# Kernel tuning notes

Measured on AMD Instinct MI355X. Metric: run time of the kernel, lower is better.

## Reference

```python
import jax, jax.numpy as jnp
import numpy as np

H, KV, DH = 16, 4, 64  # num_heads, num_kv_heads, head_dim


def setup_inputs() -> dict:
    key = jax.random.key(0)
    k1, k2, k3, k4, k5 = jax.random.split(key, 5)
    B, L, D = 1, 4096, 1024
    s = 0.02
    return {
        "x": jax.random.normal(k1, (B, L, D), dtype=jnp.float32),
        "Wq": jax.random.normal(k2, (D, H * DH), dtype=jnp.float32) * s,
        "Wk": jax.random.normal(k3, (D, KV * DH), dtype=jnp.float32) * s,
        "Wv": jax.random.normal(k4, (D, KV * DH), dtype=jnp.float32) * s,
        "Wo": jax.random.normal(k5, (H * DH, D), dtype=jnp.float32) * s,
    }


def _rotate_half(t):
    t1, t2 = t[..., : DH // 2], t[..., DH // 2 :]
    return jnp.concatenate([-t2, t1], axis=-1)


def reference(x, Wq, Wk, Wv, Wo):
    B, L, D = x.shape
    G = H // KV  # query heads per kv head
    q = (x @ Wq).reshape(B, L, H, DH)
    k = (x @ Wk).reshape(B, L, KV, DH)
    v = (x @ Wv).reshape(B, L, KV, DH)

    # RoPE: inv_freq over even dims, angles duplicated across both halves
    inv_freq = 1.0 / (10000.0 ** (jnp.arange(0, DH, 2, dtype=jnp.float32) / DH))
    t = jnp.arange(L, dtype=jnp.float32)
    freqs = t[:, None] * inv_freq[None, :]                 # [L, DH/2]
    emb = jnp.concatenate([freqs, freqs], axis=-1)[None, :, None, :]  # [1,L,1,DH]
    cos, sin = jnp.cos(emb), jnp.sin(emb)
    q = q * cos + _rotate_half(q) * sin
    k = k * cos + _rotate_half(k) * sin

    # GQA: query head h attends with kv head h // G (repeat_interleave layout)
    qg = q.reshape(B, L, KV, G, DH)
    scale = DH ** -0.5
    attn = jnp.einsum("bqkgd,bskd->bkgqs", qg, k) * scale  # [B,KV,G,L,L]
    attn = jax.nn.softmax(attn, axis=-1)
    out = jnp.einsum("bkgqs,bskd->bqkgd", attn, v).reshape(B, L, H * DH)
    return out @ Wo
```

## Files before the change

### kernel.cpp

```cpp
#include <hip/hip_runtime.h>
#include <math.h>

#define L 4096
#define D 1024
#define H 16
#define KV 4
#define DH 64

typedef __attribute__((ext_vector_type(8))) short bf16x8;
typedef __attribute__((ext_vector_type(4))) float f32x4;

static __device__ __forceinline__ unsigned short f2bf(float f) {
    unsigned u = __float_as_uint(f);
    u = (u + 0x7FFF + ((u >> 16) & 1)) >> 16;
    return (unsigned short)u;
}

#define EXP2F(x) __builtin_amdgcn_exp2f(x)

#define GLD16(src, dst) \
    __builtin_amdgcn_global_load_lds((__attribute__((address_space(1))) void*)(src), \
                                     (__attribute__((address_space(3))) void*)(dst), 16, 0, 0)

__global__ __launch_bounds__(256) void prep_kernel(
        const float* __restrict__ x,  const float* __restrict__ Wq,
        const float* __restrict__ Wk, const float* __restrict__ Wv,
        const float* __restrict__ Wo,
        unsigned short* __restrict__ xb, unsigned short* __restrict__ WqkvT,
        unsigned short* __restrict__ WoT) {
    const int b = blockIdx.x, tid = threadIdx.x;
    if (b < 4096) {
        int i = (b * 256 + tid) * 4;
        float4 v = *(const float4*)&x[i];
        ushort4 o;
        o.x = f2bf(v.x); o.y = f2bf(v.y); o.z = f2bf(v.z); o.w = f2bf(v.w);
        *(ushort4*)&xb[i] = o;
        return;
    }
    __shared__ float t[32][33];
    const float* src; unsigned short* dst; int N, n0, k0;
    if (b < 5120)      { int tq = b - 4096; src = Wq; dst = WqkvT;                     N = 1024; n0 = (tq & 31) * 32; k0 = (tq >> 5) * 32; }
    else if (b < 5376) { int tq = b - 5120; src = Wk; dst = WqkvT + (size_t)1024*1024; N = 256;  n0 = (tq & 7)  * 32; k0 = (tq >> 3) * 32; }
    else if (b < 5632) { int tq = b - 5376; src = Wv; dst = WqkvT + (size_t)1280*1024; N = 256;  n0 = (tq & 7)  * 32; k0 = (tq >> 3) * 32; }
    else               { int tq = b - 5632; src = Wo; dst = WoT;                       N = 1024; n0 = (tq & 31) * 32; k0 = (tq >> 5) * 32; }
    const int tx = tid & 31, ty = tid >> 5;
    #pragma unroll
    for (int j = 0; j < 4; ++j)
        t[ty + 8 * j][tx] = src[(size_t)(k0 + ty + 8 * j) * N + n0 + tx];
    __syncthreads();
    #pragma unroll
    for (int j = 0; j < 4; ++j)
        dst[(size_t)(n0 + ty + 8 * j) * 1024 + k0 + tx] = f2bf(t[tx][ty + 8 * j]);
}

__global__ __launch_bounds__(256) void gemm_bf16(const unsigned short* __restrict__ A,
                                                 const unsigned short* __restrict__ BT,
                                                 float* __restrict__ C,
                                                 int M, int N, int K) {
    __shared__ unsigned short As[128 * 32];
    __shared__ unsigned short Bs[128 * 32];

    const int tid  = threadIdx.x;
    const int w    = tid >> 6;
    const int lane = tid & 63;
    const int c    = lane & 15;
    const int quad = lane >> 4;
    const int wy = w >> 1, wx = w & 1;
    const int row0 = blockIdx.y * 128;
    const int col0 = blockIdx.x * 128;

    const int ld_row = w * 16 + (lane >> 2);
    const int ld_col = (lane & 3) * 8;

    f32x4 acc[4][4];
    #pragma unroll
    for (int mt = 0; mt < 4; ++mt)
        #pragma unroll
        for (int nt = 0; nt < 4; ++nt)
            acc[mt][nt] = (f32x4){0.f, 0.f, 0.f, 0.f};

    for (int k0 = 0; k0 < K; k0 += 32) {
        __syncthreads();
        GLD16(&A [(size_t)(row0 + ld_row)      * K + k0 + ld_col], &As[w * 512]);
        GLD16(&A [(size_t)(row0 + ld_row + 64) * K + k0 + ld_col], &As[w * 512 + 2048]);
        GLD16(&BT[(size_t)(col0 + ld_row)      * K + k0 + ld_col], &Bs[w * 512]);
        GLD16(&BT[(size_t)(col0 + ld_row + 64) * K + k0 + ld_col], &Bs[w * 512 + 2048]);
        __syncthreads();

        bf16x8 af[4], bfr[4];
        #pragma unroll
        for (int mt = 0; mt < 4; ++mt)
            af[mt] = *(const bf16x8*)&As[(wy * 64 + mt * 16 + c) * 32 + quad * 8];
        #pragma unroll
        for (int nt = 0; nt < 4; ++nt)
            bfr[nt] = *(const bf16x8*)&Bs[(wx * 64 + nt * 16 + c) * 32 + quad * 8];

        #pragma unroll
        for (int mt = 0; mt < 4; ++mt)
            #pragma unroll
            for (int nt = 0; nt < 4; ++nt)
                acc[mt][nt] = __builtin_amdgcn_mfma_f32_16x16x32_bf16(af[mt], bfr[nt], acc[mt][nt], 0, 0, 0);
    }

    #pragma unroll
    for (int mt = 0; mt < 4; ++mt)
        #pragma unroll
        for (int nt = 0; nt < 4; ++nt)
            #pragma unroll
            for (int r = 0; r < 4; ++r)
                C[(size_t)(row0 + wy * 64 + mt * 16 + quad * 4 + r) * N
                  + col0 + wx * 64 + nt * 16 + c] = acc[mt][nt][r];
}

__global__ __launch_bounds__(256) void gemm_qkv_rope(
        const unsigned short* __restrict__ A,
        const unsigned short* __restrict__ BT,
        unsigned short* __restrict__ qb,
        unsigned short* __restrict__ kbuf,
        unsigned short* __restrict__ vbuf) {
    __shared__ unsigned short As[128 * 32];
    __shared__ unsigned short Bs[128 * 32];

    const int tid  = threadIdx.x;
    const int w    = tid >> 6;
    const int lane = tid & 63;
    const int c    = lane & 15;
    const int quad = lane >> 4;
    const int wy = w >> 1, wx = w & 1;
    const int row0 = blockIdx.y * 128;
    const int col0 = blockIdx.x * 128;

    const int ld_row = w * 16 + (lane >> 2);
    const int ld_col = (lane & 3) * 8;

    f32x4 acc[4][4];
    #pragma unroll
    for (int mt = 0; mt < 4; ++mt)
        #pragma unroll
        for (int nt = 0; nt < 4; ++nt)
            acc[mt][nt] = (f32x4){0.f, 0.f, 0.f, 0.f};

    for (int k0 = 0; k0 < 1024; k0 += 32) {
        __syncthreads();
        GLD16(&A [(size_t)(row0 + ld_row)      * 1024 + k0 + ld_col], &As[w * 512]);
        GLD16(&A [(size_t)(row0 + ld_row + 64) * 1024 + k0 + ld_col], &As[w * 512 + 2048]);
        GLD16(&BT[(size_t)(col0 + ld_row)      * 1024 + k0 + ld_col], &Bs[w * 512]);
        GLD16(&BT[(size_t)(col0 + ld_row + 64) * 1024 + k0 + ld_col], &Bs[w * 512 + 2048]);
        __syncthreads();

        bf16x8 af[4], bfr[4];
        #pragma unroll
        for (int mt = 0; mt < 4; ++mt)
            af[mt] = *(const bf16x8*)&As[(wy * 64 + mt * 16 + c) * 32 + quad * 8];
        #pragma unroll
        for (int nt = 0; nt < 4; ++nt)
            bfr[nt] = *(const bf16x8*)&Bs[(wx * 64 + nt * 16 + c) * 32 + quad * 8];

        #pragma unroll
        for (int mt = 0; mt < 4; ++mt)
            #pragma unroll
            for (int nt = 0; nt < 4; ++nt)
                acc[mt][nt] = __builtin_amdgcn_mfma_f32_16x16x32_bf16(af[mt], bfr[nt], acc[mt][nt], 0, 0, 0);
    }

    const int colb = col0 + wx * 64;
    if (colb < 1280) {
        unsigned short* dst; int hh, hstride; float scale;
        if (colb < 1024) { dst = qb;   hh = colb >> 6;          hstride = H;  scale = 0.18033688011112042f; }
        else             { dst = kbuf; hh = (colb - 1024) >> 6; hstride = KV; scale = 1.0f; }
        #pragma unroll
        for (int nt = 0; nt < 2; ++nt) {
            int d = nt * 16 + c;
            float invf = EXP2F((float)d * -0.4152410118609203f);
            #pragma unroll
            for (int mt = 0; mt < 4; ++mt)
                #pragma unroll
                for (int r = 0; r < 4; ++r) {
                    int l = row0 + wy * 64 + mt * 16 + quad * 4 + r;
                    float ang = (float)l * invf;
                    float sn = __sinf(ang), cs = __cosf(ang);
                    float x1 = acc[mt][nt][r], x2 = acc[mt][nt + 2][r];
                    dst[((size_t)l * hstride + hh) * DH + d]      = f2bf((x1 * cs - x2 * sn) * scale);
                    dst[((size_t)l * hstride + hh) * DH + d + 32] = f2bf((x2 * cs + x1 * sn) * scale);
                }
        }
    } else {
        int vh = (colb - 1280) >> 6;
        #pragma unroll
        for (int mt = 0; mt < 4; ++mt)
            #pragma unroll
            for (int nt = 0; nt < 4; ++nt)
                #pragma unroll
                for (int r = 0; r < 4; ++r) {
                    int l = row0 + wy * 64 + mt * 16 + quad * 4 + r;
                    vbuf[((size_t)l * KV + vh) * DH + nt * 16 + c] = f2bf(acc[mt][nt][r]);
                }
    }
}

__global__ __launch_bounds__(512, 2) void attn_mfma_kernel(
        const unsigned short* __restrict__ qb,
        const unsigned short* __restrict__ kb,
        const unsigned short* __restrict__ vb,
        unsigned short* __restrict__ ob) {
    __shared__ __align__(16) unsigned short Vt[2][2][64][64];
    __shared__ __align__(16) unsigned short Ps[8][64][64];

    const int tid  = threadIdx.x;
    const int w    = tid >> 6;
    const int lane = tid & 63;
    const int c    = lane & 15;
    const int quad = lane >> 4;
    const int g    = w >> 2;
    const int kv = blockIdx.y;
    const int h  = kv * 4 + (w & 3);
    const int q0 = blockIdx.x * 64;
    const int s_base = g * 2048;

    bf16x8 qfrag[4][2];
    #pragma unroll
    for (int qt = 0; qt < 4; ++qt)
        #pragma unroll
        for (int kt = 0; kt < 2; ++kt)
            qfrag[qt][kt] = *(const bf16x8*)&qb[((size_t)(q0 + qt * 16 + c) * H + h) * DH
                                                + kt * 32 + quad * 8];

    f32x4 oacc[4][4];
    f32x4 oones[4];
    #pragma unroll
    for (int qt = 0; qt < 4; ++qt) {
        oones[qt] = (f32x4){0.f, 0.f, 0.f, 0.f};
        #pragma unroll
        for (int dt = 0; dt < 4; ++dt)
            oacc[qt][dt] = (f32x4){0.f, 0.f, 0.f, 0.f};
    }
    const short one_bf = (short)0x3F80;
    const bf16x8 ones8 = {one_bf, one_bf, one_bf, one_bf, one_bf, one_bf, one_bf, one_bf};

    const int tid8 = tid & 255;
    const int sp = tid8 & 31, dc = tid8 >> 5;
    unsigned short* PsW = &Ps[w][0][0];
    const int xr = c & 7;

    int4 vreg0 = *(const int4*)&vb[((size_t)(s_base + 2 * sp)     * KV + kv) * DH + dc * 8];
    int4 vreg1 = *(const int4*)&vb[((size_t)(s_base + 2 * sp + 1) * KV + kv) * DH + dc * 8];
    bf16x8 kA[4][2], kB[4][2];
    #pragma unroll
    for (int mt = 0; mt < 4; ++mt)
        #pragma unroll
        for (int kt = 0; kt < 2; ++kt)
            kA[mt][kt] = *(const bf16x8*)&kb[((size_t)(s_base + mt * 16 + c) * KV + kv) * DH + kt * 32 + quad * 8];

    auto step = [&](int it, int buf, bf16x8 kc[4][2], bf16x8 kn[4][2]) {
        {
            const unsigned* pa = (const unsigned*)&vreg0;
            const unsigned* pb = (const unsigned*)&vreg1;
            #pragma unroll
            for (int t = 0; t < 4; ++t) {
                unsigned lo = __builtin_amdgcn_perm(pb[t], pa[t], 0x05040100u);
                unsigned hi = __builtin_amdgcn_perm(pb[t], pa[t], 0x07060302u);
                int dl = dc * 8 + 2 * t, dh = dl + 1;
                *(unsigned*)&Vt[g][buf][dl][(((sp >> 2) ^ (dl & 7)) << 3) + 2 * (sp & 3)] = lo;
                *(unsigned*)&Vt[g][buf][dh][(((sp >> 2) ^ (dh & 7)) << 3) + 2 * (sp & 3)] = hi;
            }
        }
        __syncthreads();

        int s1 = s_base + ((it + 1) & 31) * 64;
        vreg0 = *(const int4*)&vb[((size_t)(s1 + 2 * sp)     * KV + kv) * DH + dc * 8];
        vreg1 = *(const int4*)&vb[((size_t)(s1 + 2 * sp + 1) * KV + kv) * DH + dc * 8];
        #pragma unroll
        for (int mt = 0; mt < 4; ++mt)
            #pragma unroll
            for (int kt = 0; kt < 2; ++kt)
                kn[mt][kt] = *(const bf16x8*)&kb[((size_t)(s1 + mt * 16 + c) * KV + kv) * DH + kt * 32 + quad * 8];

        #pragma unroll
        for (int mt = 0; mt < 4; ++mt) {
            f32x4 st[4];
            #pragma unroll
            for (int qt = 0; qt < 4; ++qt) {
                f32x4 a = (f32x4){0.f, 0.f, 0.f, 0.f};
                a = __builtin_amdgcn_mfma_f32_16x16x32_bf16(kc[mt][0], qfrag[qt][0], a, 0, 0, 0);
                a = __builtin_amdgcn_mfma_f32_16x16x32_bf16(kc[mt][1], qfrag[qt][1], a, 0, 0, 0);
                st[qt] = a;
            }
            #pragma unroll
            for (int qt = 0; qt < 4; ++qt) {
                float p0 = EXP2F(st[qt][0]);
                float p1 = EXP2F(st[qt][1]);
                float p2 = EXP2F(st[qt][2]);
                float p3 = EXP2F(st[qt][3]);
                uint2 pk;
                pk.x = __builtin_amdgcn_perm(__float_as_uint(p1), __float_as_uint(p0), 0x07060302u);
                pk.y = __builtin_amdgcn_perm(__float_as_uint(p3), __float_as_uint(p2), 0x07060302u);
                *(uint2*)&PsW[(qt * 16 + c) * 64 + (((2 * mt + (quad >> 1)) ^ xr) << 3) + (quad & 1) * 4] = pk;
            }
        }

        bf16x8 pf[4][2];
        #pragma unroll
        for (int qt = 0; qt < 4; ++qt)
            #pragma unroll
            for (int kt = 0; kt < 2; ++kt)
                pf[qt][kt] = *(const bf16x8*)&PsW[(qt * 16 + c) * 64 + (((kt * 4 + quad) ^ xr) << 3)];

        #pragma unroll
        for (int dt = 0; dt < 4; ++dt) {
            bf16x8 vf0 = *(const bf16x8*)&Vt[g][buf][dt * 16 + c][((0 * 4 + quad) ^ xr) << 3];
            bf16x8 vf1 = *(const bf16x8*)&Vt[g][buf][dt * 16 + c][((1 * 4 + quad) ^ xr) << 3];
            #pragma unroll
            for (int qt = 0; qt < 4; ++qt) {
                oacc[qt][dt] = __builtin_amdgcn_mfma_f32_16x16x32_bf16(pf[qt][0], vf0, oacc[qt][dt], 0, 0, 0);
                oacc[qt][dt] = __builtin_amdgcn_mfma_f32_16x16x32_bf16(pf[qt][1], vf1, oacc[qt][dt], 0, 0, 0);
            }
        }
        #pragma unroll
        for (int qt = 0; qt < 4; ++qt) {
            oones[qt] = __builtin_amdgcn_mfma_f32_16x16x32_bf16(pf[qt][0], ones8, oones[qt], 0, 0, 0);
            oones[qt] = __builtin_amdgcn_mfma_f32_16x16x32_bf16(pf[qt][1], ones8, oones[qt], 0, 0, 0);
        }
    };

    for (int it = 0; it < 32; it += 2) {
        step(it,     0, kA, kB);
        step(it + 1, 1, kB, kA);
    }

    __syncthreads();
    if (g == 1) {
        float* dsto = (float*)&Ps[0][0][0] + (size_t)(w - 4) * 4096 + lane * 64;
        #pragma unroll
        for (int qt = 0; qt < 4; ++qt)
            #pragma unroll
            for (int dt = 0; dt < 4; ++dt)
                *(f32x4*)&dsto[qt * 16 + dt * 4] = oacc[qt][dt];
        float* dsts = (float*)&Vt[0][0][0][0] + (size_t)(w - 4) * 1024 + lane * 16;
        #pragma unroll
        for (int qt = 0; qt < 4; ++qt)
            *(f32x4*)&dsts[qt * 4] = oones[qt];
    }
    __syncthreads();
    if (g == 0) {
        const float* srco = (const float*)&Ps[0][0][0] + (size_t)w * 4096 + lane * 64;
        const float* srcs = (const float*)&Vt[0][0][0][0] + (size_t)w * 1024 + lane * 16;
        #pragma unroll
        for (int qt = 0; qt < 4; ++qt) {
            f32x4 po = *(const f32x4*)&srcs[qt * 4];
            oones[qt] += po;
            #pragma unroll
            for (int dt = 0; dt < 4; ++dt)
                oacc[qt][dt] += *(const f32x4*)&srco[qt * 16 + dt * 4];
        }
        #pragma unroll
        for (int qt = 0; qt < 4; ++qt)
            #pragma unroll
            for (int r = 0; r < 4; ++r) {
                float inv = 1.0f / oones[qt][r];
                int row = q0 + qt * 16 + quad * 4 + r;
                #pragma unroll
                for (int dt = 0; dt < 4; ++dt)
                    ob[(size_t)row * (H * DH) + h * DH + dt * 16 + c] = f2bf(oacc[qt][dt][r] * inv);
            }
    }
}

extern "C" void kernel_launch(void* const* d_in, const int* in_sizes, int n_in,
                              void* d_out, int out_size, void* d_ws, size_t ws_size,
                              hipStream_t stream) {
    const float* x  = (const float*)d_in[0];
    const float* Wq = (const float*)d_in[1];
    const float* Wk = (const float*)d_in[2];
    const float* Wv = (const float*)d_in[3];
    const float* Wo = (const float*)d_in[4];
    float* out = (float*)d_out;

    char* ws = (char*)d_ws;
    unsigned short* xb    = (unsigned short*)ws;
    unsigned short* ob    = xb;
    unsigned short* qb    = (unsigned short*)(ws + 8388608);
    unsigned short* kb    = (unsigned short*)(ws + 16777216);
    unsigned short* vb    = (unsigned short*)(ws + 18874368);
    unsigned short* WqkvT = (unsigned short*)(ws + 20971520);
    unsigned short* WoT   = (unsigned short*)(ws + 24117248);

    dim3 blk(256);

    prep_kernel<<<6656, blk, 0, stream>>>(x, Wq, Wk, Wv, Wo, xb, WqkvT, WoT);

    gemm_qkv_rope<<<dim3(12, 32), blk, 0, stream>>>(xb, WqkvT, qb, kb, vb);

    attn_mfma_kernel<<<dim3(L / 64, KV), dim3(512), 0, stream>>>(qb, kb, vb, ob);

    gemm_bf16<<<dim3(D / 128, L / 128), blk, 0, stream>>>(ob, WoT, out, L, D, D);
}
```

Before: 230.0 us.

## Switch attention to 32x32x16 MFMA with register-resident P via permlane32 swap

Rewrites the attention inner loop to use 32x32x16 bf16 MFMA tiles instead of 16x16x32. The exp'd scores are converted to the PV operand layout in registers with permlane32_swap, so the per-wave LDS round trip for P goes away. Row sums are now accumulated with scalar adds instead of extra MFMAs against a ones vector. It also adds s_setprio around the PV MFMAs and reworks the cross-group reduction with a swizzled float LDS buffer. The trade-off is higher register pressure from the 16-wide accumulators, and the softmax denominators are built from truncated bf16 values so they match the numerators used in PV.

```diff
diff --git a/kernel.cpp b/kernel.cpp
--- a/kernel.cpp
+++ b/kernel.cpp
@@ -9,6 +9,8 @@
 
 typedef __attribute__((ext_vector_type(8))) short bf16x8;
 typedef __attribute__((ext_vector_type(4))) float f32x4;
+typedef __attribute__((ext_vector_type(16))) float f32x16;
+typedef __attribute__((ext_vector_type(2))) unsigned int u32x2;
 
 static __device__ __forceinline__ unsigned short f2bf(float f) {
     unsigned u = __float_as_uint(f);
@@ -16,7 +18,14 @@
     return (unsigned short)u;
 }
 
+static __device__ __forceinline__ bf16x8 mk8(unsigned a, unsigned b, unsigned c, unsigned d) {
+    union { unsigned u[4]; bf16x8 v; } x;
+    x.u[0] = a; x.u[1] = b; x.u[2] = c; x.u[3] = d;
+    return x.v;
+}
+
 #define EXP2F(x) __builtin_amdgcn_exp2f(x)
+#define ZERO16 ((f32x16){0.f,0.f,0.f,0.f,0.f,0.f,0.f,0.f,0.f,0.f,0.f,0.f,0.f,0.f,0.f,0.f})
 
 #define GLD16(src, dst) \
     __builtin_amdgcn_global_load_lds((__attribute__((address_space(1))) void*)(src), \
@@ -204,163 +213,183 @@
         const unsigned short* __restrict__ vb,
         unsigned short* __restrict__ ob) {
     __shared__ __align__(16) unsigned short Vt[2][2][64][64];
-    __shared__ __align__(16) unsigned short Ps[8][64][64];
+    __shared__ __align__(16) float Ep[4][64][64];
+    __shared__ __align__(16) float Rs[8][2][32];
 
     const int tid  = threadIdx.x;
     const int w    = tid >> 6;
     const int lane = tid & 63;
-    const int c    = lane & 15;
-    const int quad = lane >> 4;
+    const int c32  = lane & 31;
+    const int hi   = lane >> 5;
     const int g    = w >> 2;
     const int kv = blockIdx.y;
     const int h  = kv * 4 + (w & 3);
     const int q0 = blockIdx.x * 64;
     const int s_base = g * 2048;
 
-    bf16x8 qfrag[4][2];
-    #pragma unroll
-    for (int qt = 0; qt < 4; ++qt)
-        #pragma unroll
-        for (int kt = 0; kt < 2; ++kt)
-            qfrag[qt][kt] = *(const bf16x8*)&qb[((size_t)(q0 + qt * 16 + c) * H + h) * DH
-                                                + kt * 32 + quad * 8];
-
-    f32x4 oacc[4][4];
-    f32x4 oones[4];
-    #pragma unroll
-    for (int qt = 0; qt < 4; ++qt) {
-        oones[qt] = (f32x4){0.f, 0.f, 0.f, 0.f};
-        #pragma unroll
-        for (int dt = 0; dt < 4; ++dt)
-            oacc[qt][dt] = (f32x4){0.f, 0.f, 0.f, 0.f};
-    }
-    const short one_bf = (short)0x3F80;
-    const bf16x8 ones8 = {one_bf, one_bf, one_bf, one_bf, one_bf, one_bf, one_bf, one_bf};
+    bf16x8 qf[2][4];
+    {
+        const unsigned short* qbase = qb + ((size_t)(q0 + c32) * H + h) * DH + hi * 8;
+        #pragma unroll
+        for (int qt = 0; qt < 2; ++qt)
+            #pragma unroll
+            for (int kd = 0; kd < 4; ++kd)
+                qf[qt][kd] = *(const bf16x8*)&qbase[qt * 32 * H * DH + kd * 16];
+    }
+
+    f32x16 oacc[2][2];
+    #pragma unroll
+    for (int qt = 0; qt < 2; ++qt)
+        #pragma unroll
+        for (int dt = 0; dt < 2; ++dt)
+            oacc[qt][dt] = ZERO16;
+    float rsum[2] = {0.f, 0.f};
 
     const int tid8 = tid & 255;
     const int sp = tid8 & 31, dc = tid8 >> 5;
-    unsigned short* PsW = &Ps[w][0][0];
-    const int xr = c & 7;
-
-    int4 vreg0 = *(const int4*)&vb[((size_t)(s_base + 2 * sp)     * KV + kv) * DH + dc * 8];
-    int4 vreg1 = *(const int4*)&vb[((size_t)(s_base + 2 * sp + 1) * KV + kv) * DH + dc * 8];
-    bf16x8 kA[4][2], kB[4][2];
-    #pragma unroll
-    for (int mt = 0; mt < 4; ++mt)
-        #pragma unroll
-        for (int kt = 0; kt < 2; ++kt)
-            kA[mt][kt] = *(const bf16x8*)&kb[((size_t)(s_base + mt * 16 + c) * KV + kv) * DH + kt * 32 + quad * 8];
-
-    auto step = [&](int it, int buf, bf16x8 kc[4][2], bf16x8 kn[4][2]) {
+
+    const unsigned short* kbase = kb + ((size_t)(s_base + c32) * KV + kv) * DH + hi * 8;
+    const unsigned short* vbase = vb + ((size_t)(s_base + 2 * sp) * KV + kv) * DH + dc * 8;
+
+    int4 vreg0 = *(const int4*)&vbase[0];
+    int4 vreg1 = *(const int4*)&vbase[KV * DH];
+    bf16x8 kf[2][4];
+    #pragma unroll
+    for (int a = 0; a < 2; ++a)
+        #pragma unroll
+        for (int kd = 0; kd < 4; ++kd)
+            kf[a][kd] = *(const bf16x8*)&kbase[a * 32 * KV * DH + kd * 16];
+
+    auto step = [&](int it, int buf) {
         {
             const unsigned* pa = (const unsigned*)&vreg0;
             const unsigned* pb = (const unsigned*)&vreg1;
             #pragma unroll
             for (int t = 0; t < 4; ++t) {
                 unsigned lo = __builtin_amdgcn_perm(pb[t], pa[t], 0x05040100u);
-                unsigned hi = __builtin_amdgcn_perm(pb[t], pa[t], 0x07060302u);
-                int dl = dc * 8 + 2 * t, dh = dl + 1;
-                *(unsigned*)&Vt[g][buf][dl][(((sp >> 2) ^ (dl & 7)) << 3) + 2 * (sp & 3)] = lo;
-                *(unsigned*)&Vt[g][buf][dh][(((sp >> 2) ^ (dh & 7)) << 3) + 2 * (sp & 3)] = hi;
+                unsigned hv = __builtin_amdgcn_perm(pb[t], pa[t], 0x07060302u);
+                int dl = dc * 8 + 2 * t, dh2 = dl + 1;
+                *(unsigned*)&Vt[g][buf][dl ][(((sp >> 2) ^ (dl  & 7)) << 3) + 2 * (sp & 3)] = lo;
+                *(unsigned*)&Vt[g][buf][dh2][(((sp >> 2) ^ (dh2 & 7)) << 3) + 2 * (sp & 3)] = hv;
             }
         }
         __syncthreads();
 
-        int s1 = s_base + ((it + 1) & 31) * 64;
-        vreg0 = *(const int4*)&vb[((size_t)(s1 + 2 * sp)     * KV + kv) * DH + dc * 8];
-        vreg1 = *(const int4*)&vb[((size_t)(s1 + 2 * sp + 1) * KV + kv) * DH + dc * 8];
-        #pragma unroll
-        for (int mt = 0; mt < 4; ++mt)
-            #pragma unroll
-            for (int kt = 0; kt < 2; ++kt)
-                kn[mt][kt] = *(const bf16x8*)&kb[((size_t)(s1 + mt * 16 + c) * KV + kv) * DH + kt * 32 + quad * 8];
-
-        #pragma unroll
-        for (int mt = 0; mt < 4; ++mt) {
-            f32x4 st[4];
-            #pragma unroll
-            for (int qt = 0; qt < 4; ++qt) {
-                f32x4 a = (f32x4){0.f, 0.f, 0.f, 0.f};
-                a = __builtin_amdgcn_mfma_f32_16x16x32_bf16(kc[mt][0], qfrag[qt][0], a, 0, 0, 0);
-                a = __builtin_amdgcn_mfma_f32_16x16x32_bf16(kc[mt][1], qfrag[qt][1], a, 0, 0, 0);
-                st[qt] = a;
-            }
-            #pragma unroll
-            for (int qt = 0; qt < 4; ++qt) {
-                float p0 = EXP2F(st[qt][0]);
-                float p1 = EXP2F(st[qt][1]);
-                float p2 = EXP2F(st[qt][2]);
-                float p3 = EXP2F(st[qt][3]);
-                uint2 pk;
-                pk.x = __builtin_amdgcn_perm(__float_as_uint(p1), __float_as_uint(p0), 0x07060302u);
-                pk.y = __builtin_amdgcn_perm(__float_as_uint(p3), __float_as_uint(p2), 0x07060302u);
-                *(uint2*)&PsW[(qt * 16 + c) * 64 + (((2 * mt + (quad >> 1)) ^ xr) << 3) + (quad & 1) * 4] = pk;
-            }
-        }
-
-        bf16x8 pf[4][2];
-        #pragma unroll
-        for (int qt = 0; qt < 4; ++qt)
-            #pragma unroll
-            for (int kt = 0; kt < 2; ++kt)
-                pf[qt][kt] = *(const bf16x8*)&PsW[(qt * 16 + c) * 64 + (((kt * 4 + quad) ^ xr) << 3)];
-
-        #pragma unroll
-        for (int dt = 0; dt < 4; ++dt) {
-            bf16x8 vf0 = *(const bf16x8*)&Vt[g][buf][dt * 16 + c][((0 * 4 + quad) ^ xr) << 3];
-            bf16x8 vf1 = *(const bf16x8*)&Vt[g][buf][dt * 16 + c][((1 * 4 + quad) ^ xr) << 3];
-            #pragma unroll
-            for (int qt = 0; qt < 4; ++qt) {
-                oacc[qt][dt] = __builtin_amdgcn_mfma_f32_16x16x32_bf16(pf[qt][0], vf0, oacc[qt][dt], 0, 0, 0);
-                oacc[qt][dt] = __builtin_amdgcn_mfma_f32_16x16x32_bf16(pf[qt][1], vf1, oacc[qt][dt], 0, 0, 0);
-            }
-        }
-        #pragma unroll
-        for (int qt = 0; qt < 4; ++qt) {
-            oones[qt] = __builtin_amdgcn_mfma_f32_16x16x32_bf16(pf[qt][0], ones8, oones[qt], 0, 0, 0);
-            oones[qt] = __builtin_amdgcn_mfma_f32_16x16x32_bf16(pf[qt][1], ones8, oones[qt], 0, 0, 0);
+        const int itn = (it + 1) & 31;
+        vreg0 = *(const int4*)&vbase[(size_t)itn * 64 * KV * DH];
+        vreg1 = *(const int4*)&vbase[(size_t)itn * 64 * KV * DH + KV * DH];
+
+        #pragma unroll
+        for (int kt2 = 0; kt2 < 2; ++kt2) {
+            bf16x8 pf[2][2];
+            #pragma unroll
+            for (int qt = 0; qt < 2; ++qt) {
+                f32x16 s = ZERO16;
+                #pragma unroll
+                for (int kd = 0; kd < 4; ++kd)
+                    s = __builtin_amdgcn_mfma_f32_32x32x16_bf16(kf[kt2][kd], qf[qt][kd], s, 0, 0, 0);
+                float p[16];
+                #pragma unroll
+                for (int r = 0; r < 16; ++r)
+                    p[r] = __uint_as_float(__float_as_uint(EXP2F(s[r])) & 0xFFFF0000u);
+                float t0 = (p[0] + p[1]) + (p[2] + p[3]);
+                float t1 = (p[4] + p[5]) + (p[6] + p[7]);
+                float t2 = (p[8] + p[9]) + (p[10] + p[11]);
+                float t3 = (p[12] + p[13]) + (p[14] + p[15]);
+                rsum[qt] += (t0 + t1) + (t2 + t3);
+                unsigned u[8];
+                #pragma unroll
+                for (int i = 0; i < 8; ++i)
+                    u[i] = __builtin_amdgcn_perm(__float_as_uint(p[2 * i + 1]),
+                                                 __float_as_uint(p[2 * i]), 0x07060302u);
+                #pragma unroll
+                for (int f = 0; f < 2; ++f) {
+                    u32x2 e0 = __builtin_amdgcn_permlane32_swap(u[4 * f + 0], u[4 * f + 2], false, false);
+                    u32x2 e1 = __builtin_amdgcn_permlane32_swap(u[4 * f + 1], u[4 * f + 3], false, false);
+                    pf[qt][f] = mk8(e0.x, e1.x, e0.y, e1.y);
+                }
+            }
+            if (kt2 == 1) {
+                #pragma unroll
+                for (int a = 0; a < 2; ++a)
+                    #pragma unroll
+                    for (int kd = 0; kd < 4; ++kd)
+                        kf[a][kd] = *(const bf16x8*)&kbase[((size_t)itn * 64 + a * 32) * KV * DH + kd * 16];
+            }
+            __builtin_amdgcn_s_setprio(1);
+            #pragma unroll
+            for (int dt = 0; dt < 2; ++dt)
+                #pragma unroll
+                for (int f = 0; f < 2; ++f) {
+                    bf16x8 vf = *(const bf16x8*)&Vt[g][buf][dt * 32 + c32]
+                                    [(((kt2 * 4 + f * 2 + hi) ^ (c32 & 7)) << 3)];
+                    #pragma unroll
+                    for (int qt = 0; qt < 2; ++qt)
+                        oacc[qt][dt] = __builtin_amdgcn_mfma_f32_32x32x16_bf16(pf[qt][f], vf, oacc[qt][dt], 0, 0, 0);
+                }
+            __builtin_amdgcn_s_setprio(0);
         }
     };
 
     for (int it = 0; it < 32; it += 2) {
-        step(it,     0, kA, kB);
-        step(it + 1, 1, kB, kA);
-    }
-
-    __syncthreads();
+        step(it,     0);
+        step(it + 1, 1);
+    }
+
+    #pragma unroll
+    for (int qt = 0; qt < 2; ++qt) {
+        u32x2 e = __builtin_amdgcn_permlane32_swap(__float_as_uint(rsum[qt]),
+                                                   __float_as_uint(rsum[qt]), false, false);
+        float tot = __uint_as_float(e.x) + __uint_as_float(e.y);
+        Rs[w][qt][c32] = tot;
+    }
     if (g == 1) {
-        float* dsto = (float*)&Ps[0][0][0] + (size_t)(w - 4) * 4096 + lane * 64;
-        #pragma unroll
-        for (int qt = 0; qt < 4; ++qt)
-            #pragma unroll
-            for (int dt = 0; dt < 4; ++dt)
-                *(f32x4*)&dsto[qt * 16 + dt * 4] = oacc[qt][dt];
-        float* dsts = (float*)&Vt[0][0][0][0] + (size_t)(w - 4) * 1024 + lane * 16;
-        #pragma unroll
-        for (int qt = 0; qt < 4; ++qt)
-            *(f32x4*)&dsts[qt * 4] = oones[qt];
+        #pragma unroll
+        for (int qt = 0; qt < 2; ++qt)
+            #pragma unroll
+            for (int dt = 0; dt < 2; ++dt) {
+                const int d = dt * 32 + c32;
+                #pragma unroll
+                for (int rr = 0; rr < 4; ++rr) {
+                    const int gq = (qt * 8 + 2 * rr + hi) ^ (d & 15);
+                    f32x4 val = {oacc[qt][dt][rr * 4 + 0], oacc[qt][dt][rr * 4 + 1],
+                                 oacc[qt][dt][rr * 4 + 2], oacc[qt][dt][rr * 4 + 3]};
+                    *(f32x4*)&Ep[w - 4][d][gq * 4] = val;
+                }
+            }
     }
     __syncthreads();
     if (g == 0) {
-        const float* srco = (const float*)&Ps[0][0][0] + (size_t)w * 4096 + lane * 64;
-        const float* srcs = (const float*)&Vt[0][0][0][0] + (size_t)w * 1024 + lane * 16;
-        #pragma unroll
-        for (int qt = 0; qt < 4; ++qt) {
-            f32x4 po = *(const f32x4*)&srcs[qt * 4];
-            oones[qt] += po;
-            #pragma unroll
-            for (int dt = 0; dt < 4; ++dt)
-                oacc[qt][dt] += *(const f32x4*)&srco[qt * 16 + dt * 4];
-        }
-        #pragma unroll
-        for (int qt = 0; qt < 4; ++qt)
-            #pragma unroll
-            for (int r = 0; r < 4; ++r) {
-                float inv = 1.0f / oones[qt][r];
-                int row = q0 + qt * 16 + quad * 4 + r;
-                #pragma unroll
-                for (int dt = 0; dt < 4; ++dt)
-                    ob[(size_t)row * (H * DH) + h * DH + dt * 16 + c] = f2bf(oacc[qt][dt][r] * inv);
+        #pragma unroll
+        for (int qt = 0; qt < 2; ++qt)
+            #pragma unroll
+            for (int dt = 0; dt < 2; ++dt) {
+                const int d = dt * 32 + c32;
+                #pragma unroll
+                for (int rr = 0; rr < 4; ++rr) {
+                    const int gq = (qt * 8 + 2 * rr + hi) ^ (d & 15);
+                    f32x4 val = *(const f32x4*)&Ep[w][d][gq * 4];
+                    oacc[qt][dt][rr * 4 + 0] += val[0];
+                    oacc[qt][dt][rr * 4 + 1] += val[1];
+                    oacc[qt][dt][rr * 4 + 2] += val[2];
+                    oacc[qt][dt][rr * 4 + 3] += val[3];
+                }
+            }
+        #pragma unroll
+        for (int qt = 0; qt < 2; ++qt)
+            #pragma unroll
+            for (int rr = 0; rr < 4; ++rr) {
+                f32x4 ra = *(const f32x4*)&Rs[w][qt][8 * rr + 4 * hi];
+                f32x4 rb = *(const f32x4*)&Rs[w + 4][qt][8 * rr + 4 * hi];
+                #pragma unroll
+                for (int i = 0; i < 4; ++i) {
+                    float inv = 1.0f / (ra[i] + rb[i]);
+                    int row = q0 + qt * 32 + 8 * rr + 4 * hi + i;
+                    #pragma unroll
+                    for (int dt = 0; dt < 2; ++dt)
+                        ob[(size_t)row * (H * DH) + h * DH + dt * 32 + c32] =
+                            f2bf(oacc[qt][dt][rr * 4 + i] * inv);
+                }
             }
     }
 }
```

Measured after the change: 393.1 us. +71.0%, slower.
